# Kernel optimization log

Hardware: AMD Instinct MI355X
Metric: run time of the kernel (lower is better)

## Reference

```python
import jax, jax.numpy as jnp
import numpy as np

# Faithful JAX port of RayObsGraph.forward with T=1.
# torch_geometric GraphConv(x, edge_index) with add-aggregation and no edge
# weights computes: out[i] = lin_root(x[i]) + lin_rel(sum_{(j->i) in E} x[j]),
# where lin_root has no bias and lin_rel has a bias. dense_to_sparse(adj)
# yields an edge (row j -> col i) for every nonzero adj[j, i], so the
# aggregation equals binarize(adj)^T @ x, computed batched here instead of the
# original per-sample Python loop.

GS = 128      # graph_size
OBS = 1024    # obs_dim
H = 256       # gcn_h_size
OUT = 1024    # gcn_outsize
NO = 18       # num_outputs
B = 256

def setup_inputs() -> dict:
    key = jax.random.key(0)
    ks = jax.random.split(key, 16)
    inp = {
        "flat": jax.random.normal(ks[0], (B, OBS), jnp.float32),
        "nodes": jax.random.normal(ks[1], (B, GS, OBS), jnp.float32),
        "num_nodes": jax.random.randint(ks[2], (B,), 0, GS),
        "adj": jax.random.randint(ks[3], (B, GS, GS), 0, 2),
        "seq_lens": jnp.ones((B,), jnp.int32),
        # GraphConv 0: lin_rel (bias) + lin_root (no bias)
        "W0_rel": jax.random.normal(ks[4], (OBS, H), jnp.float32) / np.sqrt(OBS),
        "b0": jnp.zeros((H,), jnp.float32),
        "W0_root": jax.random.normal(ks[5], (OBS, H), jnp.float32) / np.sqrt(OBS),
        # GraphConv 1
        "W1_rel": jax.random.normal(ks[6], (H, OUT), jnp.float32) / np.sqrt(H),
        "b1": jnp.zeros((OUT,), jnp.float32),
        "W1_root": jax.random.normal(ks[7], (H, OUT), jnp.float32) / np.sqrt(H),
        # logit / value branches (SlimFC, activation None)
        "Wl": jax.random.normal(ks[8], (OUT, NO), jnp.float32) / np.sqrt(OUT),
        "bl": jnp.zeros((NO,), jnp.float32),
        "Wv": jax.random.normal(ks[9], (OUT, 1), jnp.float32) / np.sqrt(OUT),
        "bv": jnp.zeros((1,), jnp.float32),
    }
    return inp

def _forward(flat, nodes, adj, num_nodes,
             W0_rel, b0, W0_root, W1_rel, b1, W1_root, Wl, bl, Wv, bv):
    bsz = flat.shape[0]
    bi = jnp.arange(bsz)
    n = num_nodes
    nm1 = jnp.maximum(n - 1, 0)
    has_prev = n > 0

    # dense_to_sparse treats any nonzero entry as an edge (weight unused)
    A = (adj != 0).astype(flat.dtype)                       # [B, GS, GS]
    A = A.at[bi, n, n].set(1.0)
    A = A.at[bi, n, nm1].set(jnp.where(has_prev, 1.0, A[bi, n, nm1]))
    A = A.at[bi, nm1, n].set(jnp.where(has_prev, 1.0, A[bi, nm1, n]))

    # write current observation into node slot num_nodes
    x = nodes.at[bi, n].set(flat)                           # [B, GS, OBS]

    At = jnp.swapaxes(A, 1, 2)                              # message j->i: A^T
    aggr0 = jnp.einsum('bij,bjd->bid', At, x)               # [B, GS, OBS]
    h0 = jax.nn.relu(aggr0 @ W0_rel + b0 + x @ W0_root)     # [B, GS, H]
    aggr1 = jnp.einsum('bij,bjd->bid', At, h0)              # [B, GS, H]
    h1 = jax.nn.relu(aggr1 @ W1_rel + b1 + h0 @ W1_root)    # [B, GS, OUT]

    node_out = h1[bi, n]                                    # [B, OUT]
    logits = node_out @ Wl + bl                             # [B, NO]
    values = (node_out @ Wv + bv).squeeze(-1)               # [B]
    return logits, values

def reference(flat, nodes, num_nodes, adj, seq_lens,
              W0_rel, b0, W0_root, W1_rel, b1, W1_root, Wl, bl, Wv, bv):
    # seq_lens only determines B = len(seq_lens); T = flat.shape[0] // B = 1
    del seq_lens
    return _forward(flat, nodes, adj, num_nodes,
                    W0_rel, b0, W0_root, W1_rel, b1, W1_root, Wl, bl, Wv, bv)
```

## Files before the change

kernel.cpp:

```cpp
#include <hip/hip_runtime.h>
#include <hip/hip_bf16.h>
#include <cstdint>
#include <cstddef>

#define GS     128
#define OBS    1024
#define HSZ    256
#define OUTSZ  1024
#define NOUT   18
#define BATCH  256

typedef short  short8  __attribute__((ext_vector_type(8)));
typedef float  f32x4   __attribute__((ext_vector_type(4)));

__device__ __forceinline__ uint32_t f2bf_bits(float f) {
  uint32_t u = __builtin_bit_cast(uint32_t, f);
  return (u + 0x7fffu + ((u >> 16) & 1u)) >> 16;
}
__device__ __forceinline__ float bf_bits2f(uint32_t b) {
  return __builtin_bit_cast(float, b << 16);
}
__device__ __forceinline__ uint4 cvt8s(const float4 a, const float4 b) {
  float v[8] = {a.x, a.y, a.z, a.w, b.x, b.y, b.z, b.w};
  uint32_t h[8];
#pragma unroll
  for (int e = 0; e < 8; ++e) h[e] = f2bf_bits(v[e]);
  return make_uint4(h[0] | (h[1] << 16), h[2] | (h[3] << 16),
                    h[4] | (h[5] << 16), h[6] | (h[7] << 16));
}

__device__ __forceinline__ void bar_lds() {
  asm volatile("s_waitcnt lgkmcnt(0)" ::: "memory");
  __builtin_amdgcn_s_barrier();
  __builtin_amdgcn_sched_barrier(0);
}

__global__ __launch_bounds__(256) void prep_kernel(
    const float* __restrict__ W0_rel, const float* __restrict__ W0_root,
    ushort* __restrict__ WtP, const float* __restrict__ Wl,
    const float* __restrict__ Wv, float* __restrict__ WlT,
    const float* __restrict__ W1_rel, const float* __restrict__ W1_root,
    ushort* __restrict__ W1bf)
{
  __shared__ float T[64][65];
  const int blk = blockIdx.x;
  const int t = threadIdx.x;
  if (blk < 128) {
    const int k0 = (blk & 15) * 64;
    const int n0 = (blk >> 4) * 64;
    for (int idx = t; idx < 4096; idx += 256) {
      const int r = idx >> 6, c = idx & 63;
      const int n = n0 + c;
      T[r][c] = (n < HSZ) ? W0_rel[(size_t)(k0 + r) * HSZ + n]
                          : W0_root[(size_t)(k0 + r) * HSZ + (n - HSZ)];
    }
    __syncthreads();
    for (int idx = t; idx < 512; idx += 256) {
      const int nl = idx >> 3;
      const int kc = idx & 7;
      uint32_t h[8];
#pragma unroll
      for (int e = 0; e < 8; ++e) h[e] = f2bf_bits(T[kc * 8 + e][nl]);
      const int kg = k0 + kc * 8;
      const uint4 w = make_uint4(h[0] | (h[1] << 16), h[2] | (h[3] << 16),
                                 h[4] | (h[5] << 16), h[6] | (h[7] << 16));
      *(uint4*)&WtP[((size_t)((kg >> 5) * 512 + n0 + nl)) * 32 + (kg & 31)] = w;
    }
  } else if (blk < 132) {
    const int o = (blk - 128) * 256 + t;
#pragma unroll
    for (int c = 0; c < NOUT; ++c)
      WlT[(size_t)c * OUTSZ + o] = Wl[(size_t)o * NOUT + c];
    WlT[(size_t)18 * OUTSZ + o] = Wv[o];
  } else {
    const int base = (blk - 132) * 16384;
    for (int it = 0; it < 64; ++it) {
      const int idx = base + it * 256 + t;
      const int k = idx >> 10, o = idx & 1023;
      const float v = (k < HSZ) ? W1_rel[(size_t)k * OUTSZ + o]
                                : W1_root[(size_t)(k - HSZ) * OUTSZ + o];
      W1bf[idx] = (ushort)f2bf_bits(v);
    }
  }
}

__global__ __launch_bounds__(512, 2) void mega_kernel(
    const float* __restrict__ flat, const float* __restrict__ nodes,
    const int* __restrict__ num_nodes, const int* __restrict__ adj,
    const float* __restrict__ b0, const ushort* __restrict__ WtP,
    const ushort* __restrict__ W1bf, const float* __restrict__ b1,
    const float* __restrict__ WlT, const float* __restrict__ bl,
    const float* __restrict__ bv, float* __restrict__ out)
{
  __shared__ alignas(16) char smem[135168];
  ushort (*Ys)[264]     = (ushort (*)[264])smem;
  ushort (*As)[128][72] = (ushort (*)[128][72])smem;
  float  (*part)[4]     = (float  (*)[4])smem;
  __shared__ uint32_t rm[128][4];
  __shared__ uint32_t cmL[128][4];
  __shared__ float    a1s[256];
  __shared__ float    rns[256];
  __shared__ float    pl[19][4];

  const int b  = blockIdx.x;
  const int nb = num_nodes[b];
  const int t  = threadIdx.x;
  const int wv = t >> 6, lane = t & 63;
  const int ln = lane & 15, q = lane >> 4;

  {
    const int* abase = adj + ((size_t)b * GS + wv * 16) * GS;
    int va[16], vb[16];
#pragma unroll
    for (int i = 0; i < 16; ++i) {
      va[i] = abase[i * GS + lane];
      vb[i] = abase[i * GS + 64 + lane];
    }
#pragma unroll
    for (int i = 0; i < 16; ++i) {
      const int k = wv * 16 + i;
      const unsigned long long m0 = __ballot(va[i] != 0);
      const unsigned long long m1 = __ballot(vb[i] != 0);
      if (lane == 0) {
        rm[k][0] = (uint32_t)m0; rm[k][1] = (uint32_t)(m0 >> 32);
        rm[k][2] = (uint32_t)m1; rm[k][3] = (uint32_t)(m1 >> 32);
      }
    }
  }
  __syncthreads();
  if (t < 128) {
    uint32_t c0 = 0, c1 = 0, c2 = 0, c3 = 0;
    const int w = t >> 5, sh = t & 31;
#pragma unroll 8
    for (int k = 0; k < 128; ++k) {
      const uint32_t bit = (rm[k][w] >> sh) & 1u;
      if (k < 32)      c0 |= bit << k;
      else if (k < 64) c1 |= bit << (k - 32);
      else if (k < 96) c2 |= bit << (k - 64);
      else             c3 |= bit << (k - 96);
    }
    cmL[t][0] = c0; cmL[t][1] = c1; cmL[t][2] = c2; cmL[t][3] = c3;
  }
  __syncthreads();
  if (t == 0) {
    cmL[nb][nb >> 5] |= 1u << (nb & 31);
    if (nb > 0) {
      cmL[nb - 1][nb >> 5] |= 1u << (nb & 31);
      cmL[nb][(nb - 1) >> 5] |= 1u << ((nb - 1) & 31);
    }
  }

  const int arow2 = t >> 2;
  const int akb   = (t & 3) * 16;
  const float* xsrc = ((arow2 == nb) ? (flat + (size_t)b * OBS)
                                     : (nodes + ((size_t)b * GS + arow2) * OBS)) + akb;
  const ushort* bptr = WtP + ((size_t)(wv * 64 + ln)) * 32 + q * 8;

  f32x4 acc[4][8] = {};

  {
    const float4 a0 = *(const float4*)(xsrc);
    const float4 a1 = *(const float4*)(xsrc + 4);
    const float4 a2 = *(const float4*)(xsrc + 8);
    const float4 a3 = *(const float4*)(xsrc + 12);
    *(uint4*)&As[0][arow2][akb]     = cvt8s(a0, a1);
    *(uint4*)&As[0][arow2][akb + 8] = cvt8s(a2, a3);
  }
  float4 g0 = *(const float4*)(xsrc + 64);
  float4 g1 = *(const float4*)(xsrc + 68);
  float4 g2 = *(const float4*)(xsrc + 72);
  float4 g3 = *(const float4*)(xsrc + 76);
  short8 bA0 = *(const short8*)(bptr);
  short8 bA1 = *(const short8*)(bptr + 512);
  short8 bA2 = *(const short8*)(bptr + 1024);
  short8 bA3 = *(const short8*)(bptr + 1536);
  bar_lds();

  for (int s = 0; s < 16; ++s) {
    const int buf = s & 1;
    const ushort* bpB = bptr + ((size_t)(2 * s + 1)) * 16384;
    const short8 bB0 = *(const short8*)(bpB);
    const short8 bB1 = *(const short8*)(bpB + 512);
    const short8 bB2 = *(const short8*)(bpB + 1024);
    const short8 bB3 = *(const short8*)(bpB + 1536);
    short8 ah[8];
#pragma unroll
    for (int ii = 0; ii < 8; ++ii)
      ah[ii] = *(const short8*)&As[buf][ii * 16 + ln][q * 8];
#pragma unroll
    for (int ii = 0; ii < 8; ++ii) {
      acc[0][ii] = __builtin_amdgcn_mfma_f32_16x16x32_bf16(bA0, ah[ii], acc[0][ii], 0, 0, 0);
      acc[1][ii] = __builtin_amdgcn_mfma_f32_16x16x32_bf16(bA1, ah[ii], acc[1][ii], 0, 0, 0);
      acc[2][ii] = __builtin_amdgcn_mfma_f32_16x16x32_bf16(bA2, ah[ii], acc[2][ii], 0, 0, 0);
      acc[3][ii] = __builtin_amdgcn_mfma_f32_16x16x32_bf16(bA3, ah[ii], acc[3][ii], 0, 0, 0);
    }
    short8 ah2[8];
#pragma unroll
    for (int ii = 0; ii < 8; ++ii)
      ah2[ii] = *(const short8*)&As[buf][ii * 16 + ln][32 + q * 8];
    if (s + 1 < 16) {
      *(uint4*)&As[buf ^ 1][arow2][akb]     = cvt8s(g0, g1);
      *(uint4*)&As[buf ^ 1][arow2][akb + 8] = cvt8s(g2, g3);
    }
    short8 nA0 = {}, nA1 = {}, nA2 = {}, nA3 = {};
    if (s + 1 < 16) {
      const ushort* bpA = bptr + ((size_t)(2 * s + 2)) * 16384;
      nA0 = *(const short8*)(bpA);
      nA1 = *(const short8*)(bpA + 512);
      nA2 = *(const short8*)(bpA + 1024);
      nA3 = *(const short8*)(bpA + 1536);
    }
    if (s + 2 < 16) {
      g0 = *(const float4*)(xsrc + (s + 2) * 64);
      g1 = *(const float4*)(xsrc + (s + 2) * 64 + 4);
      g2 = *(const float4*)(xsrc + (s + 2) * 64 + 8);
      g3 = *(const float4*)(xsrc + (s + 2) * 64 + 12);
    }
#pragma unroll
    for (int ii = 0; ii < 8; ++ii) {
      acc[0][ii] = __builtin_amdgcn_mfma_f32_16x16x32_bf16(bB0, ah2[ii], acc[0][ii], 0, 0, 0);
      acc[1][ii] = __builtin_amdgcn_mfma_f32_16x16x32_bf16(bB1, ah2[ii], acc[1][ii], 0, 0, 0);
      acc[2][ii] = __builtin_amdgcn_mfma_f32_16x16x32_bf16(bB2, ah2[ii], acc[2][ii], 0, 0, 0);
      acc[3][ii] = __builtin_amdgcn_mfma_f32_16x16x32_bf16(bB3, ah2[ii], acc[3][ii], 0, 0, 0);
    }
    bA0 = nA0; bA1 = nA1; bA2 = nA2; bA3 = nA3;
    bar_lds();
  }

#pragma unroll
  for (int jj = 0; jj < 4; ++jj) {
    const int cat = wv * 64 + jj * 16 + q * 4;
    const int h   = cat & 255;
    const int kof = (cat < 256) ? 0 : 128;
#pragma unroll
    for (int ii = 0; ii < 8; ++ii) {
      const int kk = kof + ii * 16 + ln;
#pragma unroll
      for (int r = 0; r < 4; ++r)
        Ys[h + r][kk] = (ushort)f2bf_bits(acc[jj][ii][r]);
    }
  }
  __syncthreads();

  f32x4 acc2[8][2] = {};
#pragma unroll
  for (int ks = 0; ks < 4; ++ks) {
    const short8 bf0 = *(const short8*)&Ys[wv * 32 + ln][ks * 32 + q * 8];
    const short8 bf1 = *(const short8*)&Ys[wv * 32 + 16 + ln][ks * 32 + q * 8];
#pragma unroll
    for (int jt = 0; jt < 8; ++jt) {
      const uint32_t w = cmL[jt * 16 + ln][ks];
      const uint32_t byte_ = (w >> (q * 8)) & 0xFFu;
      short8 af;
#pragma unroll
      for (int i = 0; i < 8; ++i)
        af[i] = (short)(((byte_ >> i) & 1u) ? 0x3F80 : 0);
      acc2[jt][0] = __builtin_amdgcn_mfma_f32_16x16x32_bf16(af, bf0, acc2[jt][0], 0, 0, 0);
      acc2[jt][1] = __builtin_amdgcn_mfma_f32_16x16x32_bf16(af, bf1, acc2[jt][1], 0, 0, 0);
    }
  }

  const uint32_t S0 = cmL[nb][0], S1 = cmL[nb][1],
                 S2 = cmL[nb][2], S3 = cmL[nb][3];
  const float bb0 = b0[wv * 32 + ln];
  const float bb1 = b0[wv * 32 + 16 + ln];

  float asum0 = 0.f, asum1 = 0.f;
#pragma unroll
  for (int jt = 0; jt < 8; ++jt)
#pragma unroll
    for (int r = 0; r < 4; ++r) {
      const int j = jt * 16 + q * 4 + r;
      const uint32_t Sw = (j < 32) ? S0 : (j < 64) ? S1 : (j < 96) ? S2 : S3;
      const bool sj = (Sw >> (j & 31)) & 1u;
      const bool isn = (j == nb);
      {
        const int hl = wv * 32 + ln;
        const float yroot = bf_bits2f(Ys[hl][128 + j]);
        const float v = fmaxf(bb0 + yroot + acc2[jt][0][r], 0.f);
        if (sj) asum0 += v;
        if (isn) rns[hl] = v;
      }
      {
        const int hl = wv * 32 + 16 + ln;
        const float yroot = bf_bits2f(Ys[hl][128 + j]);
        const float v = fmaxf(bb1 + yroot + acc2[jt][1][r], 0.f);
        if (sj) asum1 += v;
        if (isn) rns[hl] = v;
      }
    }
  asum0 += __shfl_down(asum0, 32);
  asum0 += __shfl_down(asum0, 16);
  asum1 += __shfl_down(asum1, 32);
  asum1 += __shfl_down(asum1, 16);
  if (q == 0) {
    a1s[wv * 32 + ln]      = asum0;
    a1s[wv * 32 + 16 + ln] = asum1;
  }
  __syncthreads();

  const int oh = t >> 8;
  const int o4 = (t & 255) * 4;
  float4 a = make_float4(0.f, 0.f, 0.f, 0.f);
  if (oh == 0) a = *(const float4*)&b1[o4];
  const ushort* wp = W1bf + (size_t)oh * 256 * OUTSZ + o4;
  const float* sv = oh ? rns : a1s;
#pragma unroll 8
  for (int k = 0; k < 256; ++k) {
    const ushort4 w4 = *(const ushort4*)(wp + (size_t)k * OUTSZ);
    const float s = sv[k];
    a.x = fmaf(s, bf_bits2f(w4.x), a.x);
    a.y = fmaf(s, bf_bits2f(w4.y), a.y);
    a.z = fmaf(s, bf_bits2f(w4.z), a.z);
    a.w = fmaf(s, bf_bits2f(w4.w), a.w);
  }
  if (oh == 1) *(float4*)&part[t & 255][0] = a;
  __syncthreads();
  if (oh == 0) {
    const float4 pb = *(const float4*)&part[t & 255][0];
    a.x = fmaxf(a.x + pb.x, 0.f);
    a.y = fmaxf(a.y + pb.y, 0.f);
    a.z = fmaxf(a.z + pb.z, 0.f);
    a.w = fmaxf(a.w + pb.w, 0.f);
    float p[19];
#pragma unroll
    for (int c = 0; c < 19; ++c) {
      const float4 w = *(const float4*)&WlT[(size_t)c * OUTSZ + o4];
      p[c] = a.x * w.x + a.y * w.y + a.z * w.z + a.w * w.w;
    }
#pragma unroll
    for (int c = 0; c < 19; ++c) {
      float v = p[c];
      v += __shfl_down(v, 32); v += __shfl_down(v, 16);
      v += __shfl_down(v, 8);  v += __shfl_down(v, 4);
      v += __shfl_down(v, 2);  v += __shfl_down(v, 1);
      if (lane == 0) pl[c][wv] = v;
    }
  }
  __syncthreads();
  if (t < 19) {
    const float s = pl[t][0] + pl[t][1] + pl[t][2] + pl[t][3];
    if (t < NOUT) out[(size_t)b * NOUT + t] = s + bl[t];
    else          out[(size_t)BATCH * NOUT + b] = s + bv[0];
  }
}

extern "C" void kernel_launch(void* const* d_in, const int* in_sizes, int n_in,
                              void* d_out, int out_size, void* d_ws, size_t ws_size,
                              hipStream_t stream)
{
  const float* flat      = (const float*)d_in[0];
  const float* nodes     = (const float*)d_in[1];
  const int*   num_nodes = (const int*)  d_in[2];
  const int*   adj       = (const int*)  d_in[3];
  const float* W0_rel    = (const float*)d_in[5];
  const float* b0        = (const float*)d_in[6];
  const float* W0_root   = (const float*)d_in[7];
  const float* W1_rel    = (const float*)d_in[8];
  const float* b1        = (const float*)d_in[9];
  const float* W1_root   = (const float*)d_in[10];
  const float* Wl        = (const float*)d_in[11];
  const float* bl        = (const float*)d_in[12];
  const float* Wv        = (const float*)d_in[13];
  const float* bv        = (const float*)d_in[14];
  float* out = (float*)d_out;

  char* ws = (char*)d_ws;
  ushort* WtP  = (ushort*)ws;  ws += (size_t)512 * OBS * 2;
  float*  WlT  = (float*)ws;   ws += (size_t)19 * OUTSZ * 4;
  ushort* W1bf = (ushort*)ws;  ws += (size_t)512 * OUTSZ * 2;

  prep_kernel<<<164, 256, 0, stream>>>(
      W0_rel, W0_root, WtP, Wl, Wv, WlT, W1_rel, W1_root, W1bf);
  mega_kernel<<<BATCH, 512, 0, stream>>>(
      flat, nodes, num_nodes, adj, b0, WtP, W1bf, b1, WlT, bl, bv, out);
}
```

Baseline: 292.9 us.

## Double block size to 1024 threads, halving per-wave tile work

The fused per-sample kernel now launches 1024 threads (16 waves) per block instead of 512. Each wave covers 32 output columns of the first GEMM instead of 64, and 16 hidden rows instead of 32 in the aggregation. The later GEMV and logit stages are re-split over the extra threads accordingly. The aim is more waves to hide memory latency and lower per-thread register pressure. In exchange, B fragments are no longer prefetched across iterations, and the larger block with heavy LDS use still allows only one block per CU.

```diff
diff --git a/kernel.cpp b/kernel.cpp
--- a/kernel.cpp
+++ b/kernel.cpp
@@ -84,7 +84,7 @@
   }
 }
 
-__global__ __launch_bounds__(512, 2) void mega_kernel(
+__global__ __launch_bounds__(1024, 4) void mega_kernel(
     const float* __restrict__ flat, const float* __restrict__ nodes,
     const int* __restrict__ num_nodes, const int* __restrict__ adj,
     const float* __restrict__ b0, const ushort* __restrict__ WtP,
@@ -94,13 +94,13 @@
 {
   __shared__ alignas(16) char smem[135168];
   ushort (*Ys)[264]     = (ushort (*)[264])smem;
-  ushort (*As)[128][72] = (ushort (*)[128][72])smem;
-  float  (*part)[4]     = (float  (*)[4])smem;
+  ushort (*As2)[128][72] = (ushort (*)[128][72])smem;
+  float  (*part)[2]     = (float  (*)[2])smem;
   __shared__ uint32_t rm[128][4];
   __shared__ uint32_t cmL[128][4];
   __shared__ float    a1s[256];
   __shared__ float    rns[256];
-  __shared__ float    pl[19][4];
+  __shared__ float    pl[19][8];
 
   const int b  = blockIdx.x;
   const int nb = num_nodes[b];
@@ -109,16 +109,16 @@
   const int ln = lane & 15, q = lane >> 4;
 
   {
-    const int* abase = adj + ((size_t)b * GS + wv * 16) * GS;
-    int va[16], vb[16];
-#pragma unroll
-    for (int i = 0; i < 16; ++i) {
+    const int* abase = adj + ((size_t)b * GS + wv * 8) * GS;
+    int va[8], vb[8];
+#pragma unroll
+    for (int i = 0; i < 8; ++i) {
       va[i] = abase[i * GS + lane];
       vb[i] = abase[i * GS + 64 + lane];
     }
 #pragma unroll
-    for (int i = 0; i < 16; ++i) {
-      const int k = wv * 16 + i;
+    for (int i = 0; i < 8; ++i) {
+      const int k = wv * 8 + i;
       const unsigned long long m0 = __ballot(va[i] != 0);
       const unsigned long long m1 = __ballot(vb[i] != 0);
       if (lane == 0) {
@@ -150,86 +150,58 @@
     }
   }
 
-  const int arow2 = t >> 2;
-  const int akb   = (t & 3) * 16;
-  const float* xsrc = ((arow2 == nb) ? (flat + (size_t)b * OBS)
-                                     : (nodes + ((size_t)b * GS + arow2) * OBS)) + akb;
-  const ushort* bptr = WtP + ((size_t)(wv * 64 + ln)) * 32 + q * 8;
-
-  f32x4 acc[4][8] = {};
+  const int arow = t >> 3;
+  const int akb  = (t & 7) * 8;
+  const float* xsrc = ((arow == nb) ? (flat + (size_t)b * OBS)
+                                    : (nodes + ((size_t)b * GS + arow) * OBS)) + akb;
+  const ushort* bptr = WtP + ((size_t)(wv * 32 + ln)) * 32 + q * 8;
+
+  f32x4 acc[2][8] = {};
 
   {
-    const float4 a0 = *(const float4*)(xsrc);
-    const float4 a1 = *(const float4*)(xsrc + 4);
-    const float4 a2 = *(const float4*)(xsrc + 8);
-    const float4 a3 = *(const float4*)(xsrc + 12);
-    *(uint4*)&As[0][arow2][akb]     = cvt8s(a0, a1);
-    *(uint4*)&As[0][arow2][akb + 8] = cvt8s(a2, a3);
+    const float4 c0 = *(const float4*)(xsrc);
+    const float4 c1 = *(const float4*)(xsrc + 4);
+    *(uint4*)&As2[0][arow][akb] = cvt8s(c0, c1);
   }
   float4 g0 = *(const float4*)(xsrc + 64);
   float4 g1 = *(const float4*)(xsrc + 68);
-  float4 g2 = *(const float4*)(xsrc + 72);
-  float4 g3 = *(const float4*)(xsrc + 76);
-  short8 bA0 = *(const short8*)(bptr);
-  short8 bA1 = *(const short8*)(bptr + 512);
-  short8 bA2 = *(const short8*)(bptr + 1024);
-  short8 bA3 = *(const short8*)(bptr + 1536);
+  float4 g2 = *(const float4*)(xsrc + 128);
+  float4 g3 = *(const float4*)(xsrc + 132);
   bar_lds();
 
   for (int s = 0; s < 16; ++s) {
     const int buf = s & 1;
-    const ushort* bpB = bptr + ((size_t)(2 * s + 1)) * 16384;
+    const ushort* bpA = bptr + (size_t)(2 * s) * 16384;
+    const short8 bA0 = *(const short8*)(bpA);
+    const short8 bA1 = *(const short8*)(bpA + 512);
+    const ushort* bpB = bptr + (size_t)(2 * s + 1) * 16384;
     const short8 bB0 = *(const short8*)(bpB);
     const short8 bB1 = *(const short8*)(bpB + 512);
-    const short8 bB2 = *(const short8*)(bpB + 1024);
-    const short8 bB3 = *(const short8*)(bpB + 1536);
-    short8 ah[8];
-#pragma unroll
-    for (int ii = 0; ii < 8; ++ii)
-      ah[ii] = *(const short8*)&As[buf][ii * 16 + ln][q * 8];
 #pragma unroll
     for (int ii = 0; ii < 8; ++ii) {
-      acc[0][ii] = __builtin_amdgcn_mfma_f32_16x16x32_bf16(bA0, ah[ii], acc[0][ii], 0, 0, 0);
-      acc[1][ii] = __builtin_amdgcn_mfma_f32_16x16x32_bf16(bA1, ah[ii], acc[1][ii], 0, 0, 0);
-      acc[2][ii] = __builtin_amdgcn_mfma_f32_16x16x32_bf16(bA2, ah[ii], acc[2][ii], 0, 0, 0);
-      acc[3][ii] = __builtin_amdgcn_mfma_f32_16x16x32_bf16(bA3, ah[ii], acc[3][ii], 0, 0, 0);
-    }
-    short8 ah2[8];
-#pragma unroll
-    for (int ii = 0; ii < 8; ++ii)
-      ah2[ii] = *(const short8*)&As[buf][ii * 16 + ln][32 + q * 8];
-    if (s + 1 < 16) {
-      *(uint4*)&As[buf ^ 1][arow2][akb]     = cvt8s(g0, g1);
-      *(uint4*)&As[buf ^ 1][arow2][akb + 8] = cvt8s(g2, g3);
-    }
-    short8 nA0 = {}, nA1 = {}, nA2 = {}, nA3 = {};
-    if (s + 1 < 16) {
-      const ushort* bpA = bptr + ((size_t)(2 * s + 2)) * 16384;
-      nA0 = *(const short8*)(bpA);
-      nA1 = *(const short8*)(bpA + 512);
-      nA2 = *(const short8*)(bpA + 1024);
-      nA3 = *(const short8*)(bpA + 1536);
-    }
-    if (s + 2 < 16) {
-      g0 = *(const float4*)(xsrc + (s + 2) * 64);
-      g1 = *(const float4*)(xsrc + (s + 2) * 64 + 4);
-      g2 = *(const float4*)(xsrc + (s + 2) * 64 + 8);
-      g3 = *(const float4*)(xsrc + (s + 2) * 64 + 12);
+      const short8 ah = *(const short8*)&As2[buf][ii * 16 + ln][q * 8];
+      acc[0][ii] = __builtin_amdgcn_mfma_f32_16x16x32_bf16(bA0, ah, acc[0][ii], 0, 0, 0);
+      acc[1][ii] = __builtin_amdgcn_mfma_f32_16x16x32_bf16(bA1, ah, acc[1][ii], 0, 0, 0);
+    }
+    if (s + 1 < 16)
+      *(uint4*)&As2[buf ^ 1][arow][akb] = cvt8s(g0, g1);
+    g0 = g2; g1 = g3;
+    if (s + 3 < 16) {
+      g2 = *(const float4*)(xsrc + (s + 3) * 64);
+      g3 = *(const float4*)(xsrc + (s + 3) * 64 + 4);
     }
 #pragma unroll
     for (int ii = 0; ii < 8; ++ii) {
-      acc[0][ii] = __builtin_amdgcn_mfma_f32_16x16x32_bf16(bB0, ah2[ii], acc[0][ii], 0, 0, 0);
-      acc[1][ii] = __builtin_amdgcn_mfma_f32_16x16x32_bf16(bB1, ah2[ii], acc[1][ii], 0, 0, 0);
-      acc[2][ii] = __builtin_amdgcn_mfma_f32_16x16x32_bf16(bB2, ah2[ii], acc[2][ii], 0, 0, 0);
-      acc[3][ii] = __builtin_amdgcn_mfma_f32_16x16x32_bf16(bB3, ah2[ii], acc[3][ii], 0, 0, 0);
-    }
-    bA0 = nA0; bA1 = nA1; bA2 = nA2; bA3 = nA3;
+      const short8 ah2 = *(const short8*)&As2[buf][ii * 16 + ln][32 + q * 8];
+      acc[0][ii] = __builtin_amdgcn_mfma_f32_16x16x32_bf16(bB0, ah2, acc[0][ii], 0, 0, 0);
+      acc[1][ii] = __builtin_amdgcn_mfma_f32_16x16x32_bf16(bB1, ah2, acc[1][ii], 0, 0, 0);
+    }
     bar_lds();
   }
 
 #pragma unroll
-  for (int jj = 0; jj < 4; ++jj) {
-    const int cat = wv * 64 + jj * 16 + q * 4;
+  for (int jj = 0; jj < 2; ++jj) {
+    const int cat = wv * 32 + jj * 16 + q * 4;
     const int h   = cat & 255;
     const int kof = (cat < 256) ? 0 : 128;
 #pragma unroll
@@ -242,11 +214,10 @@
   }
   __syncthreads();
 
-  f32x4 acc2[8][2] = {};
+  f32x4 acc2[8] = {};
 #pragma unroll
   for (int ks = 0; ks < 4; ++ks) {
-    const short8 bf0 = *(const short8*)&Ys[wv * 32 + ln][ks * 32 + q * 8];
-    const short8 bf1 = *(const short8*)&Ys[wv * 32 + 16 + ln][ks * 32 + q * 8];
+    const short8 bf0 = *(const short8*)&Ys[wv * 16 + ln][ks * 32 + q * 8];
 #pragma unroll
     for (int jt = 0; jt < 8; ++jt) {
       const uint32_t w = cmL[jt * 16 + ln][ks];
@@ -255,17 +226,16 @@
 #pragma unroll
       for (int i = 0; i < 8; ++i)
         af[i] = (short)(((byte_ >> i) & 1u) ? 0x3F80 : 0);
-      acc2[jt][0] = __builtin_amdgcn_mfma_f32_16x16x32_bf16(af, bf0, acc2[jt][0], 0, 0, 0);
-      acc2[jt][1] = __builtin_amdgcn_mfma_f32_16x16x32_bf16(af, bf1, acc2[jt][1], 0, 0, 0);
+      acc2[jt] = __builtin_amdgcn_mfma_f32_16x16x32_bf16(af, bf0, acc2[jt], 0, 0, 0);
     }
   }
 
   const uint32_t S0 = cmL[nb][0], S1 = cmL[nb][1],
                  S2 = cmL[nb][2], S3 = cmL[nb][3];
-  const float bb0 = b0[wv * 32 + ln];
-  const float bb1 = b0[wv * 32 + 16 + ln];
-
-  float asum0 = 0.f, asum1 = 0.f;
+  const int hl = wv * 16 + ln;
+  const float bb0 = b0[hl];
+
+  float asum0 = 0.f;
 #pragma unroll
   for (int jt = 0; jt < 8; ++jt)
 #pragma unroll
@@ -274,59 +244,40 @@
       const uint32_t Sw = (j < 32) ? S0 : (j < 64) ? S1 : (j < 96) ? S2 : S3;
       const bool sj = (Sw >> (j & 31)) & 1u;
       const bool isn = (j == nb);
-      {
-        const int hl = wv * 32 + ln;
-        const float yroot = bf_bits2f(Ys[hl][128 + j]);
-        const float v = fmaxf(bb0 + yroot + acc2[jt][0][r], 0.f);
-        if (sj) asum0 += v;
-        if (isn) rns[hl] = v;
-      }
-      {
-        const int hl = wv * 32 + 16 + ln;
-        const float yroot = bf_bits2f(Ys[hl][128 + j]);
-        const float v = fmaxf(bb1 + yroot + acc2[jt][1][r], 0.f);
-        if (sj) asum1 += v;
-        if (isn) rns[hl] = v;
-      }
+      const float yroot = bf_bits2f(Ys[hl][128 + j]);
+      const float v = fmaxf(bb0 + yroot + acc2[jt][r], 0.f);
+      if (sj) asum0 += v;
+      if (isn) rns[hl] = v;
     }
   asum0 += __shfl_down(asum0, 32);
   asum0 += __shfl_down(asum0, 16);
-  asum1 += __shfl_down(asum1, 32);
-  asum1 += __shfl_down(asum1, 16);
-  if (q == 0) {
-    a1s[wv * 32 + ln]      = asum0;
-    a1s[wv * 32 + 16 + ln] = asum1;
-  }
-  __syncthreads();
-
-  const int oh = t >> 8;
-  const int o4 = (t & 255) * 4;
-  float4 a = make_float4(0.f, 0.f, 0.f, 0.f);
-  if (oh == 0) a = *(const float4*)&b1[o4];
-  const ushort* wp = W1bf + (size_t)oh * 256 * OUTSZ + o4;
+  if (q == 0) a1s[hl] = asum0;
+  __syncthreads();
+
+  const int oh = t >> 9;
+  const int oc = t & 511;
+  const int o2 = oc * 2;
+  float ax = 0.f, ay = 0.f;
+  if (oh == 0) { ax = b1[o2]; ay = b1[o2 + 1]; }
+  const ushort* wp = W1bf + (size_t)oh * 256 * OUTSZ + o2;
   const float* sv = oh ? rns : a1s;
 #pragma unroll 8
   for (int k = 0; k < 256; ++k) {
-    const ushort4 w4 = *(const ushort4*)(wp + (size_t)k * OUTSZ);
+    const ushort2 w2 = *(const ushort2*)(wp + (size_t)k * OUTSZ);
     const float s = sv[k];
-    a.x = fmaf(s, bf_bits2f(w4.x), a.x);
-    a.y = fmaf(s, bf_bits2f(w4.y), a.y);
-    a.z = fmaf(s, bf_bits2f(w4.z), a.z);
-    a.w = fmaf(s, bf_bits2f(w4.w), a.w);
-  }
-  if (oh == 1) *(float4*)&part[t & 255][0] = a;
+    ax = fmaf(s, bf_bits2f(w2.x), ax);
+    ay = fmaf(s, bf_bits2f(w2.y), ay);
+  }
+  if (oh == 1) { part[oc][0] = ax; part[oc][1] = ay; }
   __syncthreads();
   if (oh == 0) {
-    const float4 pb = *(const float4*)&part[t & 255][0];
-    a.x = fmaxf(a.x + pb.x, 0.f);
-    a.y = fmaxf(a.y + pb.y, 0.f);
-    a.z = fmaxf(a.z + pb.z, 0.f);
-    a.w = fmaxf(a.w + pb.w, 0.f);
+    ax = fmaxf(ax + part[oc][0], 0.f);
+    ay = fmaxf(ay + part[oc][1], 0.f);
     float p[19];
 #pragma unroll
     for (int c = 0; c < 19; ++c) {
-      const float4 w = *(const float4*)&WlT[(size_t)c * OUTSZ + o4];
-      p[c] = a.x * w.x + a.y * w.y + a.z * w.z + a.w * w.w;
+      const float2 w = *(const float2*)&WlT[(size_t)c * OUTSZ + o2];
+      p[c] = ax * w.x + ay * w.y;
     }
 #pragma unroll
     for (int c = 0; c < 19; ++c) {
@@ -339,7 +290,9 @@
   }
   __syncthreads();
   if (t < 19) {
-    const float s = pl[t][0] + pl[t][1] + pl[t][2] + pl[t][3];
+    float s = 0.f;
+#pragma unroll
+    for (int w = 0; w < 8; ++w) s += pl[t][w];
     if (t < NOUT) out[(size_t)b * NOUT + t] = s + bl[t];
     else          out[(size_t)BATCH * NOUT + b] = s + bv[0];
   }
@@ -372,6 +325,6 @@
 
   prep_kernel<<<164, 256, 0, stream>>>(
       W0_rel, W0_root, WtP, Wl, Wv, WlT, W1_rel, W1_root, W1bf);
-  mega_kernel<<<BATCH, 512, 0, stream>>>(
+  mega_kernel<<<BATCH, 1024, 0, stream>>>(
       flat, nodes, num_nodes, adj, b0, WtP, W1bf, b1, WlT, bl, bv, out);
 }
```

New measurement: 294.8 us. About the same (+0.6%).

## Split final GraphConv1 and output heads into a separate kernel

Applied to the files above, without the earlier changes.

Moves the per-sample layer-1 matvec and the logit/value heads out of the mega kernel into a new 256-thread kernel. The mega kernel now writes the aggregated and root hidden vectors to a bf16 workspace. Separately, the Wl/Wv transpose is dropped from prep, and the new kernel reads Wl with strided loads instead. The aim is to shorten the occupancy-limited mega kernel's tail and cut prep work, at the cost of an extra launch, a global round-trip, and bf16 rounding of the intermediate vectors.

```diff
diff --git a/kernel.cpp b/kernel.cpp
--- a/kernel.cpp
+++ b/kernel.cpp
@@ -37,8 +37,7 @@
 
 __global__ __launch_bounds__(256) void prep_kernel(
     const float* __restrict__ W0_rel, const float* __restrict__ W0_root,
-    ushort* __restrict__ WtP, const float* __restrict__ Wl,
-    const float* __restrict__ Wv, float* __restrict__ WlT,
+    ushort* __restrict__ WtP,
     const float* __restrict__ W1_rel, const float* __restrict__ W1_root,
     ushort* __restrict__ W1bf)
 {
@@ -66,14 +65,8 @@
                                  h[4] | (h[5] << 16), h[6] | (h[7] << 16));
       *(uint4*)&WtP[((size_t)((kg >> 5) * 512 + n0 + nl)) * 32 + (kg & 31)] = w;
     }
-  } else if (blk < 132) {
-    const int o = (blk - 128) * 256 + t;
-#pragma unroll
-    for (int c = 0; c < NOUT; ++c)
-      WlT[(size_t)c * OUTSZ + o] = Wl[(size_t)o * NOUT + c];
-    WlT[(size_t)18 * OUTSZ + o] = Wv[o];
   } else {
-    const int base = (blk - 132) * 16384;
+    const int base = (blk - 128) * 16384;
     for (int it = 0; it < 64; ++it) {
       const int idx = base + it * 256 + t;
       const int k = idx >> 10, o = idx & 1023;
@@ -88,19 +81,13 @@
     const float* __restrict__ flat, const float* __restrict__ nodes,
     const int* __restrict__ num_nodes, const int* __restrict__ adj,
     const float* __restrict__ b0, const ushort* __restrict__ WtP,
-    const ushort* __restrict__ W1bf, const float* __restrict__ b1,
-    const float* __restrict__ WlT, const float* __restrict__ bl,
-    const float* __restrict__ bv, float* __restrict__ out)
+    ushort* __restrict__ zbf)
 {
   __shared__ alignas(16) char smem[135168];
-  ushort (*Ys)[264]     = (ushort (*)[264])smem;
-  ushort (*As)[128][72] = (ushort (*)[128][72])smem;
-  float  (*part)[4]     = (float  (*)[4])smem;
+  ushort (*Ys)[264]      = (ushort (*)[264])smem;
+  ushort (*As2)[128][72] = (ushort (*)[128][72])smem;
   __shared__ uint32_t rm[128][4];
   __shared__ uint32_t cmL[128][4];
-  __shared__ float    a1s[256];
-  __shared__ float    rns[256];
-  __shared__ float    pl[19][4];
 
   const int b  = blockIdx.x;
   const int nb = num_nodes[b];
@@ -150,10 +137,10 @@
     }
   }
 
-  const int arow2 = t >> 2;
-  const int akb   = (t & 3) * 16;
-  const float* xsrc = ((arow2 == nb) ? (flat + (size_t)b * OBS)
-                                     : (nodes + ((size_t)b * GS + arow2) * OBS)) + akb;
+  const int arow = t >> 2;
+  const int akb  = (t & 3) * 16;
+  const float* xsrc = ((arow == nb) ? (flat + (size_t)b * OBS)
+                                    : (nodes + ((size_t)b * GS + arow) * OBS)) + akb;
   const ushort* bptr = WtP + ((size_t)(wv * 64 + ln)) * 32 + q * 8;
 
   f32x4 acc[4][8] = {};
@@ -163,8 +150,8 @@
     const float4 a1 = *(const float4*)(xsrc + 4);
     const float4 a2 = *(const float4*)(xsrc + 8);
     const float4 a3 = *(const float4*)(xsrc + 12);
-    *(uint4*)&As[0][arow2][akb]     = cvt8s(a0, a1);
-    *(uint4*)&As[0][arow2][akb + 8] = cvt8s(a2, a3);
+    *(uint4*)&As2[0][arow][akb]     = cvt8s(a0, a1);
+    *(uint4*)&As2[0][arow][akb + 8] = cvt8s(a2, a3);
   }
   float4 g0 = *(const float4*)(xsrc + 64);
   float4 g1 = *(const float4*)(xsrc + 68);
@@ -186,7 +173,7 @@
     short8 ah[8];
 #pragma unroll
     for (int ii = 0; ii < 8; ++ii)
-      ah[ii] = *(const short8*)&As[buf][ii * 16 + ln][q * 8];
+      ah[ii] = *(const short8*)&As2[buf][ii * 16 + ln][q * 8];
 #pragma unroll
     for (int ii = 0; ii < 8; ++ii) {
       acc[0][ii] = __builtin_amdgcn_mfma_f32_16x16x32_bf16(bA0, ah[ii], acc[0][ii], 0, 0, 0);
@@ -197,10 +184,10 @@
     short8 ah2[8];
 #pragma unroll
     for (int ii = 0; ii < 8; ++ii)
-      ah2[ii] = *(const short8*)&As[buf][ii * 16 + ln][32 + q * 8];
+      ah2[ii] = *(const short8*)&As2[buf][ii * 16 + ln][32 + q * 8];
     if (s + 1 < 16) {
-      *(uint4*)&As[buf ^ 1][arow2][akb]     = cvt8s(g0, g1);
-      *(uint4*)&As[buf ^ 1][arow2][akb + 8] = cvt8s(g2, g3);
+      *(uint4*)&As2[buf ^ 1][arow][akb]     = cvt8s(g0, g1);
+      *(uint4*)&As2[buf ^ 1][arow][akb + 8] = cvt8s(g2, g3);
     }
     short8 nA0 = {}, nA1 = {}, nA2 = {}, nA3 = {};
     if (s + 1 < 16) {
@@ -262,8 +249,9 @@
 
   const uint32_t S0 = cmL[nb][0], S1 = cmL[nb][1],
                  S2 = cmL[nb][2], S3 = cmL[nb][3];
-  const float bb0 = b0[wv * 32 + ln];
-  const float bb1 = b0[wv * 32 + 16 + ln];
+  const int hl0 = wv * 32 + ln, hl1 = hl0 + 16;
+  const float bb0 = b0[hl0];
+  const float bb1 = b0[hl1];
 
   float asum0 = 0.f, asum1 = 0.f;
 #pragma unroll
@@ -275,18 +263,16 @@
       const bool sj = (Sw >> (j & 31)) & 1u;
       const bool isn = (j == nb);
       {
-        const int hl = wv * 32 + ln;
-        const float yroot = bf_bits2f(Ys[hl][128 + j]);
+        const float yroot = bf_bits2f(Ys[hl0][128 + j]);
         const float v = fmaxf(bb0 + yroot + acc2[jt][0][r], 0.f);
         if (sj) asum0 += v;
-        if (isn) rns[hl] = v;
+        if (isn) zbf[(size_t)b * 512 + 256 + hl0] = (ushort)f2bf_bits(v);
       }
       {
-        const int hl = wv * 32 + 16 + ln;
-        const float yroot = bf_bits2f(Ys[hl][128 + j]);
+        const float yroot = bf_bits2f(Ys[hl1][128 + j]);
         const float v = fmaxf(bb1 + yroot + acc2[jt][1][r], 0.f);
         if (sj) asum1 += v;
-        if (isn) rns[hl] = v;
+        if (isn) zbf[(size_t)b * 512 + 256 + hl1] = (ushort)f2bf_bits(v);
       }
     }
   asum0 += __shfl_down(asum0, 32);
@@ -294,48 +280,69 @@
   asum1 += __shfl_down(asum1, 32);
   asum1 += __shfl_down(asum1, 16);
   if (q == 0) {
-    a1s[wv * 32 + ln]      = asum0;
-    a1s[wv * 32 + 16 + ln] = asum1;
-  }
-  __syncthreads();
-
-  const int oh = t >> 8;
-  const int o4 = (t & 255) * 4;
-  float4 a = make_float4(0.f, 0.f, 0.f, 0.f);
-  if (oh == 0) a = *(const float4*)&b1[o4];
-  const ushort* wp = W1bf + (size_t)oh * 256 * OUTSZ + o4;
-  const float* sv = oh ? rns : a1s;
+    zbf[(size_t)b * 512 + hl0] = (ushort)f2bf_bits(asum0);
+    zbf[(size_t)b * 512 + hl1] = (ushort)f2bf_bits(asum1);
+  }
+}
+
+__global__ __launch_bounds__(256) void d_kernel(
+    const ushort* __restrict__ zbf, const ushort* __restrict__ W1bf,
+    const float* __restrict__ b1, const float* __restrict__ Wl,
+    const float* __restrict__ Wv, const float* __restrict__ bl,
+    const float* __restrict__ bv, float* __restrict__ out)
+{
+  __shared__ float a1s[256];
+  __shared__ float rns[256];
+  __shared__ float pl[19][4];
+  const int b = blockIdx.x, t = threadIdx.x;
+  const int wv = t >> 6, lane = t & 63;
+
+  a1s[t] = bf_bits2f(zbf[(size_t)b * 512 + t]);
+  rns[t] = bf_bits2f(zbf[(size_t)b * 512 + 256 + t]);
+  __syncthreads();
+
+  const int o4 = t * 4;
+  float4 a = *(const float4*)&b1[o4];
+  const ushort* wp = W1bf + o4;
 #pragma unroll 8
   for (int k = 0; k < 256; ++k) {
     const ushort4 w4 = *(const ushort4*)(wp + (size_t)k * OUTSZ);
-    const float s = sv[k];
+    const float s = a1s[k];
     a.x = fmaf(s, bf_bits2f(w4.x), a.x);
     a.y = fmaf(s, bf_bits2f(w4.y), a.y);
     a.z = fmaf(s, bf_bits2f(w4.z), a.z);
     a.w = fmaf(s, bf_bits2f(w4.w), a.w);
   }
-  if (oh == 1) *(float4*)&part[t & 255][0] = a;
-  __syncthreads();
-  if (oh == 0) {
-    const float4 pb = *(const float4*)&part[t & 255][0];
-    a.x = fmaxf(a.x + pb.x, 0.f);
-    a.y = fmaxf(a.y + pb.y, 0.f);
-    a.z = fmaxf(a.z + pb.z, 0.f);
-    a.w = fmaxf(a.w + pb.w, 0.f);
-    float p[19];
-#pragma unroll
-    for (int c = 0; c < 19; ++c) {
-      const float4 w = *(const float4*)&WlT[(size_t)c * OUTSZ + o4];
-      p[c] = a.x * w.x + a.y * w.y + a.z * w.z + a.w * w.w;
-    }
-#pragma unroll
-    for (int c = 0; c < 19; ++c) {
-      float v = p[c];
-      v += __shfl_down(v, 32); v += __shfl_down(v, 16);
-      v += __shfl_down(v, 8);  v += __shfl_down(v, 4);
-      v += __shfl_down(v, 2);  v += __shfl_down(v, 1);
-      if (lane == 0) pl[c][wv] = v;
-    }
+#pragma unroll 8
+  for (int k = 0; k < 256; ++k) {
+    const ushort4 w4 = *(const ushort4*)(wp + (size_t)(256 + k) * OUTSZ);
+    const float s = rns[k];
+    a.x = fmaf(s, bf_bits2f(w4.x), a.x);
+    a.y = fmaf(s, bf_bits2f(w4.y), a.y);
+    a.z = fmaf(s, bf_bits2f(w4.z), a.z);
+    a.w = fmaf(s, bf_bits2f(w4.w), a.w);
+  }
+  const float av[4] = {fmaxf(a.x, 0.f), fmaxf(a.y, 0.f),
+                       fmaxf(a.z, 0.f), fmaxf(a.w, 0.f)};
+
+  float p[19];
+#pragma unroll
+  for (int c = 0; c < 19; ++c) {
+    float s = 0.f;
+#pragma unroll
+    for (int j = 0; j < 4; ++j) {
+      const float w = (c < NOUT) ? Wl[(size_t)(o4 + j) * NOUT + c] : Wv[o4 + j];
+      s = fmaf(av[j], w, s);
+    }
+    p[c] = s;
+  }
+#pragma unroll
+  for (int c = 0; c < 19; ++c) {
+    float v = p[c];
+    v += __shfl_down(v, 32); v += __shfl_down(v, 16);
+    v += __shfl_down(v, 8);  v += __shfl_down(v, 4);
+    v += __shfl_down(v, 2);  v += __shfl_down(v, 1);
+    if (lane == 0) pl[c][wv] = v;
   }
   __syncthreads();
   if (t < 19) {
@@ -367,11 +374,13 @@
 
   char* ws = (char*)d_ws;
   ushort* WtP  = (ushort*)ws;  ws += (size_t)512 * OBS * 2;
-  float*  WlT  = (float*)ws;   ws += (size_t)19 * OUTSZ * 4;
   ushort* W1bf = (ushort*)ws;  ws += (size_t)512 * OUTSZ * 2;
-
-  prep_kernel<<<164, 256, 0, stream>>>(
-      W0_rel, W0_root, WtP, Wl, Wv, WlT, W1_rel, W1_root, W1bf);
+  ushort* zbf  = (ushort*)ws;  ws += (size_t)BATCH * 512 * 2;
+
+  prep_kernel<<<160, 256, 0, stream>>>(
+      W0_rel, W0_root, WtP, W1_rel, W1_root, W1bf);
   mega_kernel<<<BATCH, 512, 0, stream>>>(
-      flat, nodes, num_nodes, adj, b0, WtP, W1bf, b1, WlT, bl, bv, out);
-}
+      flat, nodes, num_nodes, adj, b0, WtP, zbf);
+  d_kernel<<<BATCH, 256, 0, stream>>>(
+      zbf, W1bf, b1, Wl, Wv, bl, bv, out);
+}
```

New measurement: 308.8 us. 1.05x slower.
